# Kernel optimization log

Measured on AMD Instinct MI355X. Metric: run time of the kernel, lower is better.

The kernel has to match this reference:

```python
import jax, jax.numpy as jnp
import numpy as np

V, H, S, B = 32000, 256, 2048, 128

def setup_inputs() -> dict:
    key = jax.random.key(0)
    ks = jax.random.split(key, 12)
    s = 0.05
    return {
        "input_ids": jax.random.randint(ks[0], (B,), 0, V),
        "hidden": jax.random.normal(ks[1], (1, B, H), jnp.float32),
        "encoder_outputs": jax.random.normal(ks[2], (S, B, H), jnp.float32),
        "embedding": jax.random.normal(ks[3], (V, H), jnp.float32) * s,
        "attn_W": jax.random.normal(ks[4], (H, 2 * H), jnp.float32) * s,
        "attn_b": jax.random.normal(ks[5], (H,), jnp.float32) * s,
        "W_ih": jax.random.normal(ks[6], (3 * H, 2 * H), jnp.float32) * s,
        "W_hh": jax.random.normal(ks[7], (3 * H, H), jnp.float32) * s,
        "b_ih": jax.random.normal(ks[8], (3 * H,), jnp.float32) * s,
        "b_hh": jax.random.normal(ks[9], (3 * H,), jnp.float32) * s,
        "out_W": jax.random.normal(ks[10], (2 * H, V), jnp.float32) * s,
        "out_b": jax.random.normal(ks[11], (V,), jnp.float32) * s,
    }


def reference(input_ids, hidden, encoder_outputs, embedding, attn_W, attn_b,
              W_ih, W_hh, b_ih, b_hh, out_W, out_b):
    h = hidden[0]  # (B, H) -- last GRU hidden state
    # attn Linear(2H->H) on cat(h, enc): split weight into h-part and enc-part
    Wh = attn_W[:, :H]   # (H, H)
    We = attn_W[:, H:]   # (H, H)
    part_h = h @ Wh.T + attn_b                      # (B, H)
    part_e = jnp.einsum('sbh,kh->sbk', encoder_outputs, We)  # (S, B, H)
    # energy[b,i] = h_b . (Wh h_b + We e_ib + b)
    scores = jnp.einsum('bk,sbk->bs', h, part_e) + jnp.sum(h * part_h, axis=-1)[:, None]  # (B, S)
    attn_weights = jax.nn.softmax(scores, axis=1)   # (B, S)
    context = jnp.einsum('bs,sbh->bh', attn_weights, encoder_outputs)  # (B, H)
    embedded = embedding[input_ids]                 # (B, H) (dropout = eval no-op)
    x = jnp.concatenate([embedded, context], axis=1)  # (B, 2H)
    # single-step GRU (PyTorch gate ordering: r, z, n)
    gi = x @ W_ih.T + b_ih                          # (B, 3H)
    gh = h @ W_hh.T + b_hh                          # (B, 3H)
    r = jax.nn.sigmoid(gi[:, :H] + gh[:, :H])
    z = jax.nn.sigmoid(gi[:, H:2 * H] + gh[:, H:2 * H])
    n = jnp.tanh(gi[:, 2 * H:] + r * gh[:, 2 * H:])
    h_new = (1.0 - z) * n + z * h                   # (B, H)
    logits = jnp.concatenate([h_new, context], axis=1) @ out_W + out_b  # (B, V)
    output = jax.nn.log_softmax(logits, axis=1)
    return output, h_new[None], attn_weights[:, None, :]
```

## Files before the change

### kernel.cpp

```cpp
#include <hip/hip_runtime.h>

#define V 32000
#define H 256
#define S 2048
#define B 128
#define NC 64
#define CS 32

__global__ __launch_bounds__(256) void k_u(const float* __restrict__ hid,
                                           const float* __restrict__ attn_W,
                                           float* __restrict__ u) {
    __shared__ float hl[H];
    int b = blockIdx.x, t = threadIdx.x;
    hl[t] = hid[b * H + t];
    __syncthreads();
    float acc = 0.f;
    for (int k = 0; k < H; ++k)
        acc += hl[k] * attn_W[k * (2 * H) + H + t];
    u[b * H + t] = acc;
}

__global__ __launch_bounds__(256) void k_scores(const float* __restrict__ enc,
                                                const float* __restrict__ u,
                                                float* __restrict__ scores,
                                                float* __restrict__ part_m,
                                                float* __restrict__ part_l,
                                                float* __restrict__ ctx_part) {
    __shared__ float encl[CS * H];
    __shared__ float ul[H];
    __shared__ float sl[CS];
    __shared__ float wx[CS];
    int b = blockIdx.x, c = blockIdx.y, t = threadIdx.x;
    ul[t] = u[b * H + t];
    int s0 = c * CS;
    for (int i = t; i < CS * (H / 4); i += 256) {
        int row = i >> 6;
        int col = (i & 63) << 2;
        float4 f = *(const float4*)(enc + ((size_t)(s0 + row) * B + b) * H + col);
        *(float4*)(encl + row * H + col) = f;
    }
    __syncthreads();
    int w = t >> 6, l = t & 63;
    for (int j = 0; j < 8; ++j) {
        int s = w * 8 + j;
        float4 e = *(const float4*)(encl + s * H + l * 4);
        float4 uu = *(const float4*)(ul + l * 4);
        float v = e.x * uu.x + e.y * uu.y + e.z * uu.z + e.w * uu.w;
        for (int off = 32; off; off >>= 1) v += __shfl_xor(v, off, 64);
        if (l == 0) {
            sl[s] = v;
            scores[(size_t)b * S + s0 + s] = v;
        }
    }
    __syncthreads();
    if (t < CS) {
        float m = sl[t];
        for (int off = 16; off; off >>= 1) m = fmaxf(m, __shfl_xor(m, off, 64));
        m = __shfl(m, 0, 64);
        float e = __expf(sl[t] - m);
        wx[t] = e;
        float lsum = e;
        for (int off = 16; off; off >>= 1) lsum += __shfl_xor(lsum, off, 64);
        if (t == 0) {
            int pc = b * NC + c;
            part_m[pc] = m;
            part_l[pc] = lsum;
        }
    }
    __syncthreads();
    float acc = 0.f;
    for (int s = 0; s < CS; ++s) acc += wx[s] * encl[s * H + t];
    ctx_part[((size_t)(b * NC + c)) * H + t] = acc;
}

__global__ __launch_bounds__(256) void k_combine(const float* __restrict__ part_m,
                                                 const float* __restrict__ part_l,
                                                 const float* __restrict__ ctx_part,
                                                 const float* __restrict__ scores,
                                                 float* __restrict__ x2,
                                                 float* __restrict__ out_attn) {
    __shared__ float wf[NC];
    __shared__ float Ms, Ls;
    int b = blockIdx.x, t = threadIdx.x;
    if (t < NC) {
        float m = part_m[b * NC + t];
        float M = m;
        for (int off = 32; off; off >>= 1) M = fmaxf(M, __shfl_xor(M, off, 64));
        M = __shfl(M, 0, 64);
        float e = __expf(m - M);
        wf[t] = e;
        float lw = e * part_l[b * NC + t];
        for (int off = 32; off; off >>= 1) lw += __shfl_xor(lw, off, 64);
        if (t == 0) { Ms = M; Ls = lw; }
    }
    __syncthreads();
    float M = Ms, invL = 1.0f / Ls;
    float acc = 0.f;
    for (int c = 0; c < NC; ++c)
        acc += wf[c] * ctx_part[((size_t)(b * NC + c)) * H + t];
    x2[b * (2 * H) + H + t] = acc * invL;
    for (int s = t; s < S; s += 256) {
        out_attn[(size_t)b * S + s] = __expf(scores[(size_t)b * S + s] - M) * invL;
    }
}

__global__ __launch_bounds__(768) void k_gru(const int* __restrict__ ids,
                                             const float* __restrict__ hid,
                                             const float* __restrict__ emb,
                                             const float* __restrict__ W_ih,
                                             const float* __restrict__ W_hh,
                                             const float* __restrict__ b_ih,
                                             const float* __restrict__ b_hh,
                                             float* __restrict__ x2,
                                             float* __restrict__ out_h) {
    __shared__ float xl[2 * H];
    __shared__ float hl[H];
    __shared__ float gis[3 * H];
    __shared__ float ghs[3 * H];
    int b = blockIdx.x, t = threadIdx.x;
    if (t < H) xl[t] = emb[(size_t)ids[b] * H + t];
    else if (t < 2 * H) xl[t] = x2[b * (2 * H) + t];
    else hl[t - 2 * H] = hid[b * H + (t - 2 * H)];
    __syncthreads();
    int w = t >> 6, l = t & 63;
    float4 xa = *(const float4*)(xl + 4 * l);
    float4 xb = *(const float4*)(xl + H + 4 * l);
    float4 ha = *(const float4*)(hl + 4 * l);
    for (int jj = 0; jj < 64; ++jj) {
        int j = w * 64 + jj;
        const float* wr = W_ih + (size_t)j * (2 * H);
        float4 w1 = *(const float4*)(wr + 4 * l);
        float4 w2 = *(const float4*)(wr + H + 4 * l);
        float vi = w1.x * xa.x + w1.y * xa.y + w1.z * xa.z + w1.w * xa.w
                 + w2.x * xb.x + w2.y * xb.y + w2.z * xb.z + w2.w * xb.w;
        const float* vr = W_hh + (size_t)j * H;
        float4 w3 = *(const float4*)(vr + 4 * l);
        float vh = w3.x * ha.x + w3.y * ha.y + w3.z * ha.z + w3.w * ha.w;
        for (int off = 32; off; off >>= 1) {
            vi += __shfl_xor(vi, off, 64);
            vh += __shfl_xor(vh, off, 64);
        }
        if (l == 0) {
            gis[j] = vi + b_ih[j];
            ghs[j] = vh + b_hh[j];
        }
    }
    __syncthreads();
    if (t < H) {
        float r = 1.f / (1.f + __expf(-(gis[t] + ghs[t])));
        float z = 1.f / (1.f + __expf(-(gis[H + t] + ghs[H + t])));
        float n = tanhf(gis[2 * H + t] + r * ghs[2 * H + t]);
        float hn = (1.f - z) * n + z * hl[t];
        out_h[b * H + t] = hn;
        x2[b * (2 * H) + t] = hn;
    }
}

#define BT 8
__global__ __launch_bounds__(256) void k_logits(const float* __restrict__ x2,
                                                const float* __restrict__ out_W,
                                                const float* __restrict__ out_b,
                                                float* __restrict__ logits) {
    int t = threadIdx.x;
    int v0 = blockIdx.x * 1024 + 4 * t;
    int b0 = blockIdx.y * BT;
    if (v0 >= V) return;
    float4 ob = *(const float4*)(out_b + v0);
    float acc[BT][4];
    for (int bb = 0; bb < BT; ++bb) {
        acc[bb][0] = ob.x; acc[bb][1] = ob.y; acc[bb][2] = ob.z; acc[bb][3] = ob.w;
    }
    for (int k = 0; k < 2 * H; k += 4) {
        float w[4][4];
        for (int ku = 0; ku < 4; ++ku) {
            float4 wv = *(const float4*)(out_W + (size_t)(k + ku) * V + v0);
            w[ku][0] = wv.x; w[ku][1] = wv.y; w[ku][2] = wv.z; w[ku][3] = wv.w;
        }
        for (int bb = 0; bb < BT; ++bb) {
            const float* xp = x2 + ((b0 + bb) << 9) + k;
            float x0 = xp[0], x1 = xp[1], xv2 = xp[2], x3 = xp[3];
            for (int jj = 0; jj < 4; ++jj)
                acc[bb][jj] += x0 * w[0][jj] + x1 * w[1][jj] + xv2 * w[2][jj] + x3 * w[3][jj];
        }
    }
    for (int bb = 0; bb < BT; ++bb) {
        float4 r = make_float4(acc[bb][0], acc[bb][1], acc[bb][2], acc[bb][3]);
        *(float4*)(logits + (size_t)(b0 + bb) * V + v0) = r;
    }
}

__global__ __launch_bounds__(256) void k_lsm_part(const float* __restrict__ logits,
                                                  float* __restrict__ pm,
                                                  float* __restrict__ pl) {
    __shared__ float wm[4];
    __shared__ float wsum[4];
    int c = blockIdx.x, b = blockIdx.y, t = threadIdx.x;
    const float* row = logits + (size_t)b * V + c * 4000;
    float m = -1e30f;
    for (int i = t; i < 4000; i += 256) m = fmaxf(m, row[i]);
    for (int off = 32; off; off >>= 1) m = fmaxf(m, __shfl_xor(m, off, 64));
    if ((t & 63) == 0) wm[t >> 6] = m;
    __syncthreads();
    float M = fmaxf(fmaxf(wm[0], wm[1]), fmaxf(wm[2], wm[3]));
    float sacc = 0.f;
    for (int i = t; i < 4000; i += 256) sacc += __expf(row[i] - M);
    for (int off = 32; off; off >>= 1) sacc += __shfl_xor(sacc, off, 64);
    if ((t & 63) == 0) wsum[t >> 6] = sacc;
    __syncthreads();
    if (t == 0) {
        pm[b * 8 + c] = M;
        pl[b * 8 + c] = wsum[0] + wsum[1] + wsum[2] + wsum[3];
    }
}

__global__ __launch_bounds__(128) void k_lsm_comb(const float* __restrict__ pm,
                                                  const float* __restrict__ pl,
                                                  float* __restrict__ Ml,
                                                  float* __restrict__ Ll) {
    int b = threadIdx.x;
    float M = -1e30f;
    for (int c = 0; c < 8; ++c) M = fmaxf(M, pm[b * 8 + c]);
    float L = 0.f;
    for (int c = 0; c < 8; ++c) L += pl[b * 8 + c] * __expf(pm[b * 8 + c] - M);
    Ml[b] = M;
    Ll[b] = logf(L);
}

__global__ __launch_bounds__(256) void k_lsm_write(const float* __restrict__ logits,
                                                   const float* __restrict__ Ml,
                                                   const float* __restrict__ Ll,
                                                   float* __restrict__ out) {
    int b = blockIdx.y, t = threadIdx.x;
    int v = blockIdx.x * 1024 + 4 * t;
    if (v >= V) return;
    float off = Ml[b] + Ll[b];
    float4 x = *(const float4*)(logits + (size_t)b * V + v);
    float4 o = make_float4(x.x - off, x.y - off, x.z - off, x.w - off);
    *(float4*)(out + (size_t)b * V + v) = o;
}

extern "C" void kernel_launch(void* const* d_in, const int* in_sizes, int n_in,
                              void* d_out, int out_size, void* d_ws, size_t ws_size,
                              hipStream_t stream) {
    const int* ids = (const int*)d_in[0];
    const float* hid = (const float*)d_in[1];
    const float* enc = (const float*)d_in[2];
    const float* emb = (const float*)d_in[3];
    const float* attn_W = (const float*)d_in[4];
    const float* W_ih = (const float*)d_in[6];
    const float* W_hh = (const float*)d_in[7];
    const float* b_ih = (const float*)d_in[8];
    const float* b_hh = (const float*)d_in[9];
    const float* out_W = (const float*)d_in[10];
    const float* out_b = (const float*)d_in[11];

    float* out = (float*)d_out;
    float* out_logprob = out;
    float* out_h = out + (size_t)B * V;
    float* out_attn = out + (size_t)B * V + B * H;

    float* w = (float*)d_ws;
    float* u        = w;
    float* scores   = w + 32768;
    float* part_m   = w + 294912;
    float* part_l   = w + 303104;
    float* ctx_part = w + 311296;
    float* x2       = w + 2408448;
    float* logits   = w + 2473984;
    float* lsm      = w + 6569984;
    float* lsl      = w + 6571008;
    float* Ml       = w + 6572032;
    float* Ll       = w + 6572160;

    hipLaunchKernelGGL(k_u, dim3(B), dim3(256), 0, stream, hid, attn_W, u);
    hipLaunchKernelGGL(k_scores, dim3(B, NC), dim3(256), 0, stream,
                       enc, u, scores, part_m, part_l, ctx_part);
    hipLaunchKernelGGL(k_combine, dim3(B), dim3(256), 0, stream,
                       part_m, part_l, ctx_part, scores, x2, out_attn);
    hipLaunchKernelGGL(k_gru, dim3(B), dim3(768), 0, stream,
                       ids, hid, emb, W_ih, W_hh, b_ih, b_hh, x2, out_h);
    hipLaunchKernelGGL(k_logits, dim3(32, 16), dim3(256), 0, stream,
                       x2, out_W, out_b, logits);
    hipLaunchKernelGGL(k_lsm_part, dim3(8, B), dim3(256), 0, stream, logits, lsm, lsl);
    hipLaunchKernelGGL(k_lsm_comb, dim3(1), dim3(128), 0, stream, lsm, lsl, Ml, Ll);
    hipLaunchKernelGGL(k_lsm_write, dim3(32, B), dim3(256), 0, stream,
                       logits, Ml, Ll, out_logprob);
}
```

Measured before the change: 650.0 us.

## Fuse log-softmax partial reductions into logits GEMM and double-buffer weight loads

```diff
diff --git a/kernel.cpp b/kernel.cpp
--- a/kernel.cpp
+++ b/kernel.cpp
@@ -156,60 +156,85 @@
     }
 }
 
-#define BT 8
+#define BT 16
+#define NVC 32
 __global__ __launch_bounds__(256) void k_logits(const float* __restrict__ x2,
                                                 const float* __restrict__ out_W,
                                                 const float* __restrict__ out_b,
-                                                float* __restrict__ logits) {
+                                                float* __restrict__ logits,
+                                                float* __restrict__ pm,
+                                                float* __restrict__ pl) {
+    __shared__ float wred[4][BT];
+    __shared__ float Ms[BT];
     int t = threadIdx.x;
     int v0 = blockIdx.x * 1024 + 4 * t;
     int b0 = blockIdx.y * BT;
-    if (v0 >= V) return;
-    float4 ob = *(const float4*)(out_b + v0);
+    bool act = v0 < V;
     float acc[BT][4];
+    if (act) {
+        float4 ob = *(const float4*)(out_b + v0);
+#pragma unroll
+        for (int bb = 0; bb < BT; ++bb) {
+            acc[bb][0] = ob.x; acc[bb][1] = ob.y; acc[bb][2] = ob.z; acc[bb][3] = ob.w;
+        }
+        float4 cw[4];
+#pragma unroll
+        for (int ku = 0; ku < 4; ++ku)
+            cw[ku] = *(const float4*)(out_W + (size_t)ku * V + v0);
+        for (int k = 0; k < 2 * H; k += 4) {
+            int kn = (k + 4 < 2 * H) ? (k + 4) : k;
+            float4 nw[4];
+#pragma unroll
+            for (int ku = 0; ku < 4; ++ku)
+                nw[ku] = *(const float4*)(out_W + (size_t)(kn + ku) * V + v0);
+#pragma unroll
+            for (int bb = 0; bb < BT; ++bb) {
+                float4 xv = *(const float4*)(x2 + ((b0 + bb) << 9) + k);
+                acc[bb][0] += xv.x * cw[0].x + xv.y * cw[1].x + xv.z * cw[2].x + xv.w * cw[3].x;
+                acc[bb][1] += xv.x * cw[0].y + xv.y * cw[1].y + xv.z * cw[2].y + xv.w * cw[3].y;
+                acc[bb][2] += xv.x * cw[0].z + xv.y * cw[1].z + xv.z * cw[2].z + xv.w * cw[3].z;
+                acc[bb][3] += xv.x * cw[0].w + xv.y * cw[1].w + xv.z * cw[2].w + xv.w * cw[3].w;
+            }
+#pragma unroll
+            for (int ku = 0; ku < 4; ++ku) cw[ku] = nw[ku];
+        }
+#pragma unroll
+        for (int bb = 0; bb < BT; ++bb) {
+            float4 r = make_float4(acc[bb][0], acc[bb][1], acc[bb][2], acc[bb][3]);
+            *(float4*)(logits + (size_t)(b0 + bb) * V + v0) = r;
+        }
+    } else {
+#pragma unroll
+        for (int bb = 0; bb < BT; ++bb)
+            acc[bb][0] = acc[bb][1] = acc[bb][2] = acc[bb][3] = -1e30f;
+    }
+    int wid = t >> 6, l = t & 63;
+#pragma unroll
     for (int bb = 0; bb < BT; ++bb) {
-        acc[bb][0] = ob.x; acc[bb][1] = ob.y; acc[bb][2] = ob.z; acc[bb][3] = ob.w;
-    }
-    for (int k = 0; k < 2 * H; k += 4) {
-        float w[4][4];
-        for (int ku = 0; ku < 4; ++ku) {
-            float4 wv = *(const float4*)(out_W + (size_t)(k + ku) * V + v0);
-            w[ku][0] = wv.x; w[ku][1] = wv.y; w[ku][2] = wv.z; w[ku][3] = wv.w;
-        }
-        for (int bb = 0; bb < BT; ++bb) {
-            const float* xp = x2 + ((b0 + bb) << 9) + k;
-            float x0 = xp[0], x1 = xp[1], xv2 = xp[2], x3 = xp[3];
-            for (int jj = 0; jj < 4; ++jj)
-                acc[bb][jj] += x0 * w[0][jj] + x1 * w[1][jj] + xv2 * w[2][jj] + x3 * w[3][jj];
-        }
-    }
+        float m = fmaxf(fmaxf(acc[bb][0], acc[bb][1]), fmaxf(acc[bb][2], acc[bb][3]));
+        for (int off = 32; off; off >>= 1) m = fmaxf(m, __shfl_xor(m, off, 64));
+        if (l == 0) wred[wid][bb] = m;
+    }
+    __syncthreads();
+    if (t < BT)
+        Ms[t] = fmaxf(fmaxf(wred[0][t], wred[1][t]), fmaxf(wred[2][t], wred[3][t]));
+    __syncthreads();
+#pragma unroll
     for (int bb = 0; bb < BT; ++bb) {
-        float4 r = make_float4(acc[bb][0], acc[bb][1], acc[bb][2], acc[bb][3]);
-        *(float4*)(logits + (size_t)(b0 + bb) * V + v0) = r;
-    }
-}
-
-__global__ __launch_bounds__(256) void k_lsm_part(const float* __restrict__ logits,
-                                                  float* __restrict__ pm,
-                                                  float* __restrict__ pl) {
-    __shared__ float wm[4];
-    __shared__ float wsum[4];
-    int c = blockIdx.x, b = blockIdx.y, t = threadIdx.x;
-    const float* row = logits + (size_t)b * V + c * 4000;
-    float m = -1e30f;
-    for (int i = t; i < 4000; i += 256) m = fmaxf(m, row[i]);
-    for (int off = 32; off; off >>= 1) m = fmaxf(m, __shfl_xor(m, off, 64));
-    if ((t & 63) == 0) wm[t >> 6] = m;
-    __syncthreads();
-    float M = fmaxf(fmaxf(wm[0], wm[1]), fmaxf(wm[2], wm[3]));
-    float sacc = 0.f;
-    for (int i = t; i < 4000; i += 256) sacc += __expf(row[i] - M);
-    for (int off = 32; off; off >>= 1) sacc += __shfl_xor(sacc, off, 64);
-    if ((t & 63) == 0) wsum[t >> 6] = sacc;
-    __syncthreads();
-    if (t == 0) {
-        pm[b * 8 + c] = M;
-        pl[b * 8 + c] = wsum[0] + wsum[1] + wsum[2] + wsum[3];
+        float M = Ms[bb];
+        float sacc = 0.f;
+        if (act) {
+            sacc = __expf(acc[bb][0] - M) + __expf(acc[bb][1] - M)
+                 + __expf(acc[bb][2] - M) + __expf(acc[bb][3] - M);
+        }
+        for (int off = 32; off; off >>= 1) sacc += __shfl_xor(sacc, off, 64);
+        if (l == 0) wred[wid][bb] = sacc;
+    }
+    __syncthreads();
+    if (t < BT) {
+        float L = wred[0][t] + wred[1][t] + wred[2][t] + wred[3][t];
+        pm[(b0 + t) * NVC + blockIdx.x] = Ms[t];
+        pl[(b0 + t) * NVC + blockIdx.x] = L;
     }
 }
 
@@ -219,9 +244,9 @@
                                                   float* __restrict__ Ll) {
     int b = threadIdx.x;
     float M = -1e30f;
-    for (int c = 0; c < 8; ++c) M = fmaxf(M, pm[b * 8 + c]);
+    for (int c = 0; c < NVC; ++c) M = fmaxf(M, pm[b * NVC + c]);
     float L = 0.f;
-    for (int c = 0; c < 8; ++c) L += pl[b * 8 + c] * __expf(pm[b * 8 + c] - M);
+    for (int c = 0; c < NVC; ++c) L += pl[b * NVC + c] * __expf(pm[b * NVC + c] - M);
     Ml[b] = M;
     Ll[b] = logf(L);
 }
@@ -268,9 +293,9 @@
     float* x2       = w + 2408448;
     float* logits   = w + 2473984;
     float* lsm      = w + 6569984;
-    float* lsl      = w + 6571008;
-    float* Ml       = w + 6572032;
-    float* Ll       = w + 6572160;
+    float* lsl      = w + 6574080;
+    float* Ml       = w + 6578176;
+    float* Ll       = w + 6578304;
 
     hipLaunchKernelGGL(k_u, dim3(B), dim3(256), 0, stream, hid, attn_W, u);
     hipLaunchKernelGGL(k_scores, dim3(B, NC), dim3(256), 0, stream,
@@ -279,9 +304,8 @@
                        part_m, part_l, ctx_part, scores, x2, out_attn);
     hipLaunchKernelGGL(k_gru, dim3(B), dim3(768), 0, stream,
                        ids, hid, emb, W_ih, W_hh, b_ih, b_hh, x2, out_h);
-    hipLaunchKernelGGL(k_logits, dim3(32, 16), dim3(256), 0, stream,
-                       x2, out_W, out_b, logits);
-    hipLaunchKernelGGL(k_lsm_part, dim3(8, B), dim3(256), 0, stream, logits, lsm, lsl);
+    hipLaunchKernelGGL(k_logits, dim3(32, B / BT), dim3(256), 0, stream,
+                       x2, out_W, out_b, logits, lsm, lsl);
     hipLaunchKernelGGL(k_lsm_comb, dim3(1), dim3(128), 0, stream, lsm, lsl, Ml, Ll);
     hipLaunchKernelGGL(k_lsm_write, dim3(32, B), dim3(256), 0, stream,
                        logits, Ml, Ll, out_logprob);
```

After: 671.4 us. 3.3% more time.

## Split-K logits GEMM with larger batch tile and shared-memory activations

Applied to the files above, without the earlier changes.

```diff
diff --git a/kernel.cpp b/kernel.cpp
--- a/kernel.cpp
+++ b/kernel.cpp
@@ -156,54 +156,96 @@
     }
 }
 
-#define BT 8
-__global__ __launch_bounds__(256) void k_logits(const float* __restrict__ x2,
-                                                const float* __restrict__ out_W,
-                                                const float* __restrict__ out_b,
-                                                float* __restrict__ logits) {
+#define BT2 32
+#define KH 256
+__global__ __launch_bounds__(256, 1) void k_logits(const float* __restrict__ x2,
+                                                   const float* __restrict__ out_W,
+                                                   const float* __restrict__ out_b,
+                                                   float* __restrict__ ph) {
+    __shared__ float xs[BT2 * KH];
     int t = threadIdx.x;
     int v0 = blockIdx.x * 1024 + 4 * t;
-    int b0 = blockIdx.y * BT;
+    int b0 = blockIdx.y * BT2;
+    int kh = blockIdx.z;
+    int k0 = kh * KH;
+    for (int i = t; i < BT2 * (KH / 4); i += 256) {
+        int bb = i >> 6;
+        int kk = (i & 63) << 2;
+        *(float4*)(xs + bb * KH + kk) =
+            *(const float4*)(x2 + (size_t)(b0 + bb) * (2 * H) + k0 + kk);
+    }
+    __syncthreads();
     if (v0 >= V) return;
-    float4 ob = *(const float4*)(out_b + v0);
-    float acc[BT][4];
-    for (int bb = 0; bb < BT; ++bb) {
-        acc[bb][0] = ob.x; acc[bb][1] = ob.y; acc[bb][2] = ob.z; acc[bb][3] = ob.w;
-    }
-    for (int k = 0; k < 2 * H; k += 4) {
-        float w[4][4];
-        for (int ku = 0; ku < 4; ++ku) {
-            float4 wv = *(const float4*)(out_W + (size_t)(k + ku) * V + v0);
-            w[ku][0] = wv.x; w[ku][1] = wv.y; w[ku][2] = wv.z; w[ku][3] = wv.w;
-        }
-        for (int bb = 0; bb < BT; ++bb) {
-            const float* xp = x2 + ((b0 + bb) << 9) + k;
-            float x0 = xp[0], x1 = xp[1], xv2 = xp[2], x3 = xp[3];
-            for (int jj = 0; jj < 4; ++jj)
-                acc[bb][jj] += x0 * w[0][jj] + x1 * w[1][jj] + xv2 * w[2][jj] + x3 * w[3][jj];
-        }
-    }
-    for (int bb = 0; bb < BT; ++bb) {
+
+    float acc[BT2][4];
+    if (kh == 0) {
+        float4 ob = *(const float4*)(out_b + v0);
+#pragma unroll
+        for (int bb = 0; bb < BT2; ++bb) {
+            acc[bb][0] = ob.x; acc[bb][1] = ob.y; acc[bb][2] = ob.z; acc[bb][3] = ob.w;
+        }
+    } else {
+#pragma unroll
+        for (int bb = 0; bb < BT2; ++bb)
+            acc[bb][0] = acc[bb][1] = acc[bb][2] = acc[bb][3] = 0.f;
+    }
+
+    const float* Wp = out_W + (size_t)k0 * V + v0;
+    float4 cw[4];
+#pragma unroll
+    for (int ku = 0; ku < 4; ++ku)
+        cw[ku] = *(const float4*)(Wp + (size_t)ku * V);
+    for (int k = 0; k < KH; k += 4) {
+        int kn = (k + 4 < KH) ? (k + 4) : k;
+        float4 nw[4];
+#pragma unroll
+        for (int ku = 0; ku < 4; ++ku)
+            nw[ku] = *(const float4*)(Wp + (size_t)(kn + ku) * V);
+#pragma unroll
+        for (int bb = 0; bb < BT2; ++bb) {
+            float4 xv = *(const float4*)(xs + bb * KH + k);
+            acc[bb][0] += xv.x * cw[0].x + xv.y * cw[1].x + xv.z * cw[2].x + xv.w * cw[3].x;
+            acc[bb][1] += xv.x * cw[0].y + xv.y * cw[1].y + xv.z * cw[2].y + xv.w * cw[3].y;
+            acc[bb][2] += xv.x * cw[0].z + xv.y * cw[1].z + xv.z * cw[2].z + xv.w * cw[3].z;
+            acc[bb][3] += xv.x * cw[0].w + xv.y * cw[1].w + xv.z * cw[2].w + xv.w * cw[3].w;
+        }
+#pragma unroll
+        for (int ku = 0; ku < 4; ++ku) cw[ku] = nw[ku];
+    }
+
+    float* dst = ph + (size_t)kh * B * V;
+#pragma unroll
+    for (int bb = 0; bb < BT2; ++bb) {
         float4 r = make_float4(acc[bb][0], acc[bb][1], acc[bb][2], acc[bb][3]);
-        *(float4*)(logits + (size_t)(b0 + bb) * V + v0) = r;
-    }
-}
-
-__global__ __launch_bounds__(256) void k_lsm_part(const float* __restrict__ logits,
+        *(float4*)(dst + (size_t)(b0 + bb) * V + v0) = r;
+    }
+}
+
+__global__ __launch_bounds__(256) void k_lsm_part(const float* __restrict__ ph,
                                                   float* __restrict__ pm,
                                                   float* __restrict__ pl) {
     __shared__ float wm[4];
     __shared__ float wsum[4];
     int c = blockIdx.x, b = blockIdx.y, t = threadIdx.x;
-    const float* row = logits + (size_t)b * V + c * 4000;
+    const float* r0 = ph + (size_t)b * V + c * 4000;
+    const float* r1 = ph + (size_t)(B + b) * V + c * 4000;
     float m = -1e30f;
-    for (int i = t; i < 4000; i += 256) m = fmaxf(m, row[i]);
+    for (int i = 4 * t; i < 4000; i += 1024) {
+        float4 a = *(const float4*)(r0 + i);
+        float4 q = *(const float4*)(r1 + i);
+        m = fmaxf(m, fmaxf(fmaxf(a.x + q.x, a.y + q.y), fmaxf(a.z + q.z, a.w + q.w)));
+    }
     for (int off = 32; off; off >>= 1) m = fmaxf(m, __shfl_xor(m, off, 64));
     if ((t & 63) == 0) wm[t >> 6] = m;
     __syncthreads();
     float M = fmaxf(fmaxf(wm[0], wm[1]), fmaxf(wm[2], wm[3]));
     float sacc = 0.f;
-    for (int i = t; i < 4000; i += 256) sacc += __expf(row[i] - M);
+    for (int i = 4 * t; i < 4000; i += 1024) {
+        float4 a = *(const float4*)(r0 + i);
+        float4 q = *(const float4*)(r1 + i);
+        sacc += __expf(a.x + q.x - M) + __expf(a.y + q.y - M)
+              + __expf(a.z + q.z - M) + __expf(a.w + q.w - M);
+    }
     for (int off = 32; off; off >>= 1) sacc += __shfl_xor(sacc, off, 64);
     if ((t & 63) == 0) wsum[t >> 6] = sacc;
     __syncthreads();
@@ -226,7 +268,7 @@
     Ll[b] = logf(L);
 }
 
-__global__ __launch_bounds__(256) void k_lsm_write(const float* __restrict__ logits,
+__global__ __launch_bounds__(256) void k_lsm_write(const float* __restrict__ ph,
                                                    const float* __restrict__ Ml,
                                                    const float* __restrict__ Ll,
                                                    float* __restrict__ out) {
@@ -234,8 +276,10 @@
     int v = blockIdx.x * 1024 + 4 * t;
     if (v >= V) return;
     float off = Ml[b] + Ll[b];
-    float4 x = *(const float4*)(logits + (size_t)b * V + v);
-    float4 o = make_float4(x.x - off, x.y - off, x.z - off, x.w - off);
+    float4 a = *(const float4*)(ph + (size_t)b * V + v);
+    float4 q = *(const float4*)(ph + (size_t)(B + b) * V + v);
+    float4 o = make_float4(a.x + q.x - off, a.y + q.y - off,
+                           a.z + q.z - off, a.w + q.w - off);
     *(float4*)(out + (size_t)b * V + v) = o;
 }
 
@@ -266,11 +310,11 @@
     float* part_l   = w + 303104;
     float* ctx_part = w + 311296;
     float* x2       = w + 2408448;
-    float* logits   = w + 2473984;
-    float* lsm      = w + 6569984;
-    float* lsl      = w + 6571008;
-    float* Ml       = w + 6572032;
-    float* Ll       = w + 6572160;
+    float* ph       = w + 2473984;
+    float* lsm      = w + 10665984;
+    float* lsl      = w + 10667008;
+    float* Ml       = w + 10668032;
+    float* Ll       = w + 10668160;
 
     hipLaunchKernelGGL(k_u, dim3(B), dim3(256), 0, stream, hid, attn_W, u);
     hipLaunchKernelGGL(k_scores, dim3(B, NC), dim3(256), 0, stream,
@@ -279,10 +323,10 @@
                        part_m, part_l, ctx_part, scores, x2, out_attn);
     hipLaunchKernelGGL(k_gru, dim3(B), dim3(768), 0, stream,
                        ids, hid, emb, W_ih, W_hh, b_ih, b_hh, x2, out_h);
-    hipLaunchKernelGGL(k_logits, dim3(32, 16), dim3(256), 0, stream,
-                       x2, out_W, out_b, logits);
-    hipLaunchKernelGGL(k_lsm_part, dim3(8, B), dim3(256), 0, stream, logits, lsm, lsl);
+    hipLaunchKernelGGL(k_logits, dim3(32, B / BT2, 2), dim3(256), 0, stream,
+                       x2, out_W, out_b, ph);
+    hipLaunchKernelGGL(k_lsm_part, dim3(8, B), dim3(256), 0, stream, ph, lsm, lsl);
     hipLaunchKernelGGL(k_lsm_comb, dim3(1), dim3(128), 0, stream, lsm, lsl, Ml, Ll);
     hipLaunchKernelGGL(k_lsm_write, dim3(32, B), dim3(256), 0, stream,
-                       logits, Ml, Ll, out_logprob);
-}
+                       ph, Ml, Ll, out_logprob);
+}
```

Result: no change. 650.5 us (+0.1%).
